# Kernel tuning notes

Measured on AMD Instinct MI355X. Metric: run time of the kernel, lower is better.

## Reference

```python
import jax, jax.numpy as jnp
import numpy as np

B, IN_DIM, R_DIM = 8192, 2048, 4096
LEAK_RATE = 0.3


def setup_inputs() -> dict:
    key = jax.random.key(0)
    k1, k2, k3, k4 = jax.random.split(key, 4)
    inputs = jax.random.normal(k1, (B, IN_DIM), dtype=jnp.float32)
    prev_state = jax.random.normal(k2, (B, R_DIM), dtype=jnp.float32)
    # weights scaled down for numerical sanity inside tanh
    input_weights = jax.random.normal(k3, (R_DIM, IN_DIM), dtype=jnp.float32) * 0.02
    reservoir_weights = jax.random.normal(k4, (R_DIM, R_DIM), dtype=jnp.float32) * 0.02
    return {
        "inputs": inputs,
        "prev_state": prev_state,
        "input_weights": input_weights,
        "reservoir_weights": reservoir_weights,
    }


def reference(inputs, prev_state, input_weights, reservoir_weights):
    # input_part = inputs @ input_weights.T        -> [B, R]
    # reservoir_part = prev_state @ reservoir_weights.T -> [B, R]
    input_part = jnp.einsum("bi,ri->br", inputs, input_weights)
    reservoir_part = jnp.einsum("bq,rq->br", prev_state, reservoir_weights)
    state = (1.0 - LEAK_RATE) * prev_state + LEAK_RATE * jnp.tanh(input_part + reservoir_part)
    return state
```

## Files before the change

kernel.cpp:

```cpp
#include <hip/hip_runtime.h>
#include <cstdint>
#include <cstddef>

typedef unsigned short u16;
typedef __attribute__((ext_vector_type(8))) short short8;
typedef __attribute__((ext_vector_type(16))) float f32x16;
typedef __attribute__((ext_vector_type(4))) float f32x4;
typedef __attribute__((ext_vector_type(4))) int i32x4;

constexpr int M  = 8192;
constexpr int Nn = 4096;
constexpr int K1 = 2048;
constexpr int K2 = 4096;
constexpr int K  = K1 + K2;
constexpr int BM = 256, BN = 256;
constexpr int NKT = K / 64;
constexpr int NBK = K / 64;
constexpr float LEAK = 0.3f;

__device__ __forceinline__ u16 f2bf(float f) {
  unsigned u = __float_as_uint(f);
  u += 0x7FFFu + ((u >> 16) & 1u);
  return (u16)(u >> 16);
}

template<int C1, int C2>
__global__ void cast_concat_blk(const float* __restrict__ X, const float* __restrict__ S,
                                u16* __restrict__ out)
{
  __shared__ u16 tile[64 * 72];
  const int bid = blockIdx.x;
  const int t   = bid % NBK;
  const int g   = bid / NBK;
  const int tid = threadIdx.x;
  const int row = tid >> 2;
  const int cs  = (tid & 3) * 16;
  const int gcol = t * 64 + cs;
  const int grow = g * 64 + row;
  const float* src = (gcol < C1) ? (X + (size_t)grow * C1 + gcol)
                                 : (S + (size_t)grow * C2 + (gcol - C1));
  const float4* s4 = (const float4*)src;
  u16* d = tile + row * 72 + cs;
  #pragma unroll
  for (int q = 0; q < 4; ++q) {
    float4 f = s4[q];
    d[q * 4 + 0] = f2bf(f.x); d[q * 4 + 1] = f2bf(f.y);
    d[q * 4 + 2] = f2bf(f.z); d[q * 4 + 3] = f2bf(f.w);
  }
  __syncthreads();
  u16* ob = out + (size_t)bid * 4096;
  #pragma unroll
  for (int h = 0; h < 2; ++h) {
    const int s   = tid + h * 256;
    const int rb2 = s >> 8, kc = (s >> 5) & 7, r = s & 31;
    const u16* p  = tile + (rb2 * 32 + r) * 72 + kc * 8;
    *(i32x4*)(ob + s * 8) = *(const i32x4*)p;
  }
}

__device__ __forceinline__ void gload16(const u16* g, u16* l) {
  __builtin_amdgcn_global_load_lds(
      (const __attribute__((address_space(1))) void*)g,
      (__attribute__((address_space(3))) void*)l, 16, 0, 0);
}

__device__ __forceinline__ float fast_tanh(float x) {
  const float ax = __builtin_fabsf(x);
  const float e  = __builtin_amdgcn_exp2f(ax * 2.8853900817779268f);
  const float r  = 1.0f - 2.0f * __builtin_amdgcn_rcpf(e + 1.0f);
  return __builtin_copysignf(r, x);
}

#define BAR()   __builtin_amdgcn_s_barrier()
#define LGKM0() asm volatile("s_waitcnt lgkmcnt(0)" ::: "memory")
#define LGKM4() asm volatile("s_waitcnt lgkmcnt(4)" ::: "memory")
#define LGKM8() asm volatile("s_waitcnt lgkmcnt(8)" ::: "memory")
#define VMW8()  asm volatile("s_waitcnt vmcnt(8)" ::: "memory")
#define VMW0()  asm volatile("s_waitcnt vmcnt(0)" ::: "memory")
#define SB0()   __builtin_amdgcn_sched_barrier(0)

__global__ __launch_bounds__(512, 2) void gemm_fused(
    const u16* __restrict__ A,
    const u16* __restrict__ W,
    const float* __restrict__ prev,
    float* __restrict__ out)
{
  __shared__ u16 lds[69632];

  const int tid  = threadIdx.x;
  const int lane = tid & 63;
  const int wid  = tid >> 6;
  const int wr   = wid >> 2;
  const int wc   = wid & 3;

  const int cpx = gridDim.x >> 3;
  const int wg  = ((int)blockIdx.x & 7) * cpx + ((int)blockIdx.x >> 3);
  const int bn  = wg & 15;
  const int bm  = wg >> 4;

  constexpr size_t BLK = 4096;
  constexpr size_t RG  = (size_t)NBK * BLK;
  const u16* pA = A + (size_t)(4 * bm) * RG + tid * 8;
  const u16* pW = W + (size_t)(4 * bn) * RG + tid * 8;
  u16* ldsw = lds + wid * 512;

  auto stg = [&](const u16* g, int dst) {
    gload16(g,      ldsw + dst);
    gload16(g + RG, ldsw + dst + 4096);
  };

  short8 afE[2][4], afO[2][4];
  short8 bfE[4],    bfO[4];
  f32x16 acc[4][2];
  #pragma unroll
  for (int mt = 0; mt < 4; ++mt)
    #pragma unroll
    for (int ng = 0; ng < 2; ++ng) acc[mt][ng] = (f32x16)0.f;

  auto dsA = [&](short8 (&Av)[2][4], int mg, int ab) {
    #pragma unroll
    for (int mtl = 0; mtl < 2; ++mtl) {
      const int rb = wr * 4 + mg * 2 + mtl;
      #pragma unroll
      for (int ks = 0; ks < 4; ++ks)
        Av[mtl][ks] = *(const short8*)(lds + ab + rb * 2048 + ks * 512 + lane * 8);
    }
  };
  auto dsB = [&](short8 (&Bv)[4], int ng, int bb) {
    const int rb = wc * 2 + ng;
    #pragma unroll
    for (int ks = 0; ks < 4; ++ks)
      Bv[ks] = *(const short8*)(lds + bb + rb * 2048 + ks * 512 + lane * 8);
  };
  auto MM = [&](short8 (&Av)[2][4], short8 (&Bv)[4], int mg, int ng) {
    __builtin_amdgcn_s_setprio(1);
    #pragma unroll
    for (int ks = 0; ks < 4; ++ks)
      #pragma unroll
      for (int mtl = 0; mtl < 2; ++mtl)
        acc[mg * 2 + mtl][ng] = __builtin_amdgcn_mfma_f32_32x32x16_bf16(
            Av[mtl][ks], Bv[ks], acc[mg * 2 + mtl][ng], 0, 0, 0);
    __builtin_amdgcn_s_setprio(0);
  };

  stg(pW,                32768); stg(pW + 2 * RG,       32768 + 8192);
  stg(pA,                0);     stg(pA + 2 * RG,       8192);
  stg(pW + BLK,          49152); stg(pW + 2 * RG + BLK, 49152 + 8192);
  stg(pA + BLK,          16384); stg(pA + 2 * RG + BLK, 16384 + 8192);
  VMW8();
  BAR();
  dsA(afE, 0, 0);
  dsB(bfE, 0, 32768);

  const u16* gA = pA;
  const u16* gW = pW;
  #pragma unroll 1
  for (int i = 0; i < 47; ++i) {
    dsB(bfO, 1, 32768);
    LGKM4(); SB0(); MM(afE, bfE, 0, 0); BAR();
    dsA(afO, 1, 0);
    LGKM8(); SB0(); MM(afE, bfO, 0, 1); VMW0(); BAR();
    dsA(afE, 0, 16384);
    stg(gW + 2 * BLK, 32768); stg(gW + 2 * RG + 2 * BLK, 32768 + 8192);
    LGKM8(); SB0(); MM(afO, bfE, 1, 0); BAR();
    dsB(bfE, 0, 49152);
    stg(gA + 2 * BLK, 0); stg(gA + 2 * RG + 2 * BLK, 8192);
    SB0(); MM(afO, bfO, 1, 1); BAR();
    dsB(bfO, 1, 49152);
    LGKM4(); SB0(); MM(afE, bfE, 0, 0); BAR();
    dsA(afO, 1, 16384);
    LGKM8(); SB0(); MM(afE, bfO, 0, 1); VMW0(); BAR();
    dsA(afE, 0, 0);
    stg(gW + 3 * BLK, 49152); stg(gW + 2 * RG + 3 * BLK, 49152 + 8192);
    LGKM8(); SB0(); MM(afO, bfE, 1, 0); BAR();
    dsB(bfE, 0, 32768);
    stg(gA + 3 * BLK, 16384); stg(gA + 2 * RG + 3 * BLK, 16384 + 8192);
    SB0(); MM(afO, bfO, 1, 1); BAR();
    gA += 2 * BLK; gW += 2 * BLK;
  }

  dsB(bfO, 1, 32768);
  LGKM4(); SB0(); MM(afE, bfE, 0, 0); BAR();
  dsA(afO, 1, 0);
  LGKM8(); SB0(); MM(afE, bfO, 0, 1); VMW0(); BAR();
  dsA(afE, 0, 16384);
  LGKM8(); SB0(); MM(afO, bfE, 1, 0); BAR();
  dsB(bfE, 0, 49152);
  SB0(); MM(afO, bfO, 1, 1); BAR();
  dsB(bfO, 1, 49152);
  LGKM4(); SB0(); MM(afE, bfE, 0, 0); BAR();
  dsA(afO, 1, 16384);
  LGKM8(); SB0(); MM(afE, bfO, 0, 1); BAR();
  LGKM0(); SB0(); MM(afO, bfE, 1, 0);
  MM(afO, bfO, 1, 1);

  BAR();
  float* T = (float*)((char*)lds + wid * 17408);
  const int l31 = lane & 31, l5 = lane >> 5;
  const int c16 = lane & 15, g4 = lane >> 4;
  #pragma unroll
  for (int ch = 0; ch < 2; ++ch) {
    #pragma unroll
    for (int mtl = 0; mtl < 2; ++mtl)
      #pragma unroll
      for (int ng = 0; ng < 2; ++ng)
        #pragma unroll
        for (int j = 0; j < 16; ++j) {
          const int rowl = mtl * 32 + (j & 3) + 8 * (j >> 2) + l5 * 4;
          T[rowl * 68 + ng * 32 + l31] = acc[ch * 2 + mtl][ng][j];
        }
    LGKM0();
    const int grow0 = bm * BM + wr * 128 + ch * 64;
    const size_t gcb = (size_t)(bn * BN + wc * 64 + c16 * 4);
    #pragma unroll 4
    for (int q = 0; q < 16; ++q) {
      const int rowl = q * 4 + g4;
      const f32x4 t = *(const f32x4*)&T[rowl * 68 + c16 * 4];
      const size_t off = (size_t)(grow0 + rowl) * Nn + gcb;
      const f32x4 p = __builtin_nontemporal_load((const f32x4*)(prev + off));
      f32x4 o;
      o.x = (1.0f - LEAK) * p.x + LEAK * fast_tanh(t.x);
      o.y = (1.0f - LEAK) * p.y + LEAK * fast_tanh(t.y);
      o.z = (1.0f - LEAK) * p.z + LEAK * fast_tanh(t.z);
      o.w = (1.0f - LEAK) * p.w + LEAK * fast_tanh(t.w);
      __builtin_nontemporal_store(o, (f32x4*)(out + off));
    }
  }
}

extern "C" void kernel_launch(void* const* d_in, const int* in_sizes, int n_in,
                              void* d_out, int out_size, void* d_ws, size_t ws_size,
                              hipStream_t stream) {
  const float* inputs = (const float*)d_in[0];
  const float* prev   = (const float*)d_in[1];
  const float* w_in   = (const float*)d_in[2];
  const float* w_res  = (const float*)d_in[3];
  float* out = (float*)d_out;

  u16* Acat = (u16*)d_ws;
  u16* Wcat = Acat + (size_t)M * K;

  cast_concat_blk<K1, K2><<<(M / 64) * NBK, 256, 0, stream>>>(inputs, prev, Acat);
  cast_concat_blk<K1, K2><<<(Nn / 64) * NBK, 256, 0, stream>>>(w_in, w_res, Wcat);

  gemm_fused<<<(M / BM) * (Nn / BN), 512, 0, stream>>>(Acat, Wcat, prev, out);
}
```

Before: 445.3 us.

## Reschedule GEMM prefetch stages and drop redundant barriers in main loop

Restructures the software pipeline of the fused bf16 GEMM. Each operand's K-tile (four row-groups) is now loaded in a single staging call, and the A-tile prefetch is issued earlier, at the start of each half-iteration. Several workgroup barriers between MFMA phases are removed, leaving two per half-iteration. This cuts barrier stalls and gives the global-to-LDS loads more lead time, at the risk of LDS read/write races if the remaining waits and barriers do not fully cover buffer reuse.

```diff
diff --git a/kernel.cpp b/kernel.cpp
--- a/kernel.cpp
+++ b/kernel.cpp
@@ -14,7 +14,6 @@
 constexpr int K2 = 4096;
 constexpr int K  = K1 + K2;
 constexpr int BM = 256, BN = 256;
-constexpr int NKT = K / 64;
 constexpr int NBK = K / 64;
 constexpr float LEAK = 0.3f;
 
@@ -71,13 +70,13 @@
   return __builtin_copysignf(r, x);
 }
 
-#define BAR()   __builtin_amdgcn_s_barrier()
-#define LGKM0() asm volatile("s_waitcnt lgkmcnt(0)" ::: "memory")
-#define LGKM4() asm volatile("s_waitcnt lgkmcnt(4)" ::: "memory")
-#define LGKM8() asm volatile("s_waitcnt lgkmcnt(8)" ::: "memory")
-#define VMW8()  asm volatile("s_waitcnt vmcnt(8)" ::: "memory")
-#define VMW0()  asm volatile("s_waitcnt vmcnt(0)" ::: "memory")
-#define SB0()   __builtin_amdgcn_sched_barrier(0)
+#define BAR()    __builtin_amdgcn_s_barrier()
+#define LGKM0()  asm volatile("s_waitcnt lgkmcnt(0)" ::: "memory")
+#define LGKM4()  asm volatile("s_waitcnt lgkmcnt(4)" ::: "memory")
+#define LGKM8()  asm volatile("s_waitcnt lgkmcnt(8)" ::: "memory")
+#define VMW4()   asm volatile("s_waitcnt vmcnt(4)" ::: "memory")
+#define VMW0()   asm volatile("s_waitcnt vmcnt(0)" ::: "memory")
+#define SB0()    __builtin_amdgcn_sched_barrier(0)
 
 __global__ __launch_bounds__(512, 2) void gemm_fused(
     const u16* __restrict__ A,
@@ -104,9 +103,10 @@
   const u16* pW = W + (size_t)(4 * bn) * RG + tid * 8;
   u16* ldsw = lds + wid * 512;
 
-  auto stg = [&](const u16* g, int dst) {
-    gload16(g,      ldsw + dst);
-    gload16(g + RG, ldsw + dst + 4096);
+  auto stgT = [&](const u16* p, int t, int bufel) {
+    #pragma unroll
+    for (int r = 0; r < 4; ++r)
+      gload16(p + (size_t)r * RG + (size_t)t * BLK, ldsw + bufel + r * 4096);
   };
 
   short8 afE[2][4], afO[2][4];
@@ -143,54 +143,52 @@
     __builtin_amdgcn_s_setprio(0);
   };
 
-  stg(pW,                32768); stg(pW + 2 * RG,       32768 + 8192);
-  stg(pA,                0);     stg(pA + 2 * RG,       8192);
-  stg(pW + BLK,          49152); stg(pW + 2 * RG + BLK, 49152 + 8192);
-  stg(pA + BLK,          16384); stg(pA + 2 * RG + BLK, 16384 + 8192);
-  VMW8();
+  stgT(pW, 0, 32768);
+  stgT(pA, 0, 0);
+  stgT(pW, 1, 49152);
+  VMW4();
   BAR();
   dsA(afE, 0, 0);
   dsB(bfE, 0, 32768);
 
-  const u16* gA = pA;
-  const u16* gW = pW;
   #pragma unroll 1
   for (int i = 0; i < 47; ++i) {
+    const int T = 2 * i;
     dsB(bfO, 1, 32768);
-    LGKM4(); SB0(); MM(afE, bfE, 0, 0); BAR();
+    stgT(pA, T + 1, 16384);
+    LGKM4(); SB0(); MM(afE, bfE, 0, 0);
     dsA(afO, 1, 0);
     LGKM8(); SB0(); MM(afE, bfO, 0, 1); VMW0(); BAR();
     dsA(afE, 0, 16384);
-    stg(gW + 2 * BLK, 32768); stg(gW + 2 * RG + 2 * BLK, 32768 + 8192);
-    LGKM8(); SB0(); MM(afO, bfE, 1, 0); BAR();
+    stgT(pW, T + 2, 32768);
+    LGKM8(); SB0(); MM(afO, bfE, 1, 0);
     dsB(bfE, 0, 49152);
-    stg(gA + 2 * BLK, 0); stg(gA + 2 * RG + 2 * BLK, 8192);
     SB0(); MM(afO, bfO, 1, 1); BAR();
     dsB(bfO, 1, 49152);
-    LGKM4(); SB0(); MM(afE, bfE, 0, 0); BAR();
+    stgT(pA, T + 2, 0);
+    LGKM4(); SB0(); MM(afE, bfE, 0, 0);
     dsA(afO, 1, 16384);
     LGKM8(); SB0(); MM(afE, bfO, 0, 1); VMW0(); BAR();
     dsA(afE, 0, 0);
-    stg(gW + 3 * BLK, 49152); stg(gW + 2 * RG + 3 * BLK, 49152 + 8192);
-    LGKM8(); SB0(); MM(afO, bfE, 1, 0); BAR();
+    stgT(pW, T + 3, 49152);
+    LGKM8(); SB0(); MM(afO, bfE, 1, 0);
     dsB(bfE, 0, 32768);
-    stg(gA + 3 * BLK, 16384); stg(gA + 2 * RG + 3 * BLK, 16384 + 8192);
     SB0(); MM(afO, bfO, 1, 1); BAR();
-    gA += 2 * BLK; gW += 2 * BLK;
   }
 
   dsB(bfO, 1, 32768);
-  LGKM4(); SB0(); MM(afE, bfE, 0, 0); BAR();
+  stgT(pA, 95, 16384);
+  LGKM4(); SB0(); MM(afE, bfE, 0, 0);
   dsA(afO, 1, 0);
   LGKM8(); SB0(); MM(afE, bfO, 0, 1); VMW0(); BAR();
   dsA(afE, 0, 16384);
-  LGKM8(); SB0(); MM(afO, bfE, 1, 0); BAR();
+  LGKM8(); SB0(); MM(afO, bfE, 1, 0);
   dsB(bfE, 0, 49152);
   SB0(); MM(afO, bfO, 1, 1); BAR();
   dsB(bfO, 1, 49152);
-  LGKM4(); SB0(); MM(afE, bfE, 0, 0); BAR();
+  LGKM4(); SB0(); MM(afE, bfE, 0, 0);
   dsA(afO, 1, 16384);
-  LGKM8(); SB0(); MM(afE, bfO, 0, 1); BAR();
+  LGKM8(); SB0(); MM(afE, bfO, 0, 1);
   LGKM0(); SB0(); MM(afO, bfE, 1, 0);
   MM(afO, bfO, 1, 1);
 
```

After: 452.8 us. No clear change (+1.7%).
